# Kernel tuning notes

Measured on AMD Instinct MI355X. Metric: run time of the kernel, lower is better.

## Reference

```python
import jax, jax.numpy as jnp
import numpy as np

B, T, D = 32, 512, 1024
EPS = 1e-12  # torch F.normalize eps


def smooth_l1(x):
    # nn.SmoothL1Loss default beta=1.0
    a = jnp.abs(x)
    return jnp.where(a < 1.0, 0.5 * x * x, a - 0.5)


def setup_inputs() -> dict:
    key = jax.random.key(0)
    k1, k2, k3, k4 = jax.random.split(key, 4)
    return {
        "word_targets": jax.random.normal(k1, (B, T, D), dtype=jnp.float32),
        "image_targets": jax.random.normal(k2, (B, D), dtype=jnp.float32),
        "preds": jax.random.normal(k3, (B, T, D), dtype=jnp.float32),
        "decode_lengths": jax.random.randint(k4, (B,), 1, T + 1, dtype=jnp.int32),
    }


def reference(word_targets, image_targets, preds, decode_lengths):
    # mask over valid (ragged) positions: [B, T]
    mask = (jnp.arange(T)[None, :] < decode_lengths[:, None]).astype(preds.dtype)
    lens = decode_lengths.astype(preds.dtype)  # [B]

    # word loss: per-sample mean of smooth_l1 over valid tokens x D
    sl1 = smooth_l1(preds - word_targets) * mask[:, :, None]  # [B,T,D]
    word_per_b = sl1.sum(axis=(1, 2)) / (lens * D)             # [B]
    word_loss = word_per_b.mean()

    # per-sentence means over valid tokens: [B, D]
    pred_mean = (preds * mask[:, :, None]).sum(axis=1) / lens[:, None]
    targ_mean = (word_targets * mask[:, :, None]).sum(axis=1) / lens[:, None]
    sentence_loss = smooth_l1(pred_mean - targ_mean).mean(axis=1).mean()

    # image embedding loss: compare pred sentence mean to L2-normalized image embedding
    norm = jnp.maximum(jnp.linalg.norm(image_targets, axis=-1, keepdims=True), EPS)
    img_norm = image_targets / norm
    image_loss = smooth_l1(pred_mean - img_norm).mean(axis=1).mean()

    return word_loss + sentence_loss + image_loss
```

## Files before the change

kernel.cpp:

```cpp
#include <hip/hip_runtime.h>
#include <math.h>

static constexpr int B_ = 32;
static constexpr int T_ = 512;
static constexpr int D_ = 1024;
static constexpr int NT_ = 32;
static constexpr int TCHUNK_ = T_ / NT_;
static constexpr int GRID1_ = 1024;
static constexpr float EPS_ = 1e-12f;

__device__ __forceinline__ float sl1f(float x) {
    float a = fabsf(x);
    return a < 1.0f ? 0.5f * x * x : a - 0.5f;
}

__device__ __forceinline__ float blockReduce256(float v, float* lds) {
#pragma unroll
    for (int o = 32; o > 0; o >>= 1) v += __shfl_down(v, o, 64);
    int wid = threadIdx.x >> 6, lane = threadIdx.x & 63;
    if (lane == 0) lds[wid] = v;
    __syncthreads();
    float tot = lds[0] + lds[1] + lds[2] + lds[3];
    __syncthreads();
    return tot;
}

__global__ __launch_bounds__(256, 4) void pass1_kernel(
    const float* __restrict__ preds, const float* __restrict__ wtarg,
    const int* __restrict__ lens,
    float* __restrict__ wsPred, float* __restrict__ wsTarg, float* __restrict__ wsSl1,
    float* __restrict__ out)
{
    __shared__ float lds[4];
    __shared__ int sPrefix[B_ + 1];
    __shared__ int sLen[B_];

    const int tid = threadIdx.x;
    if (blockIdx.x == 0 && tid == 0) out[0] = 0.f;

    if (tid < 64) {
        int len_t = (tid < B_) ? lens[tid] : 0;
        int nc = (len_t + TCHUNK_ - 1) / TCHUNK_;
        int incl = nc;
#pragma unroll
        for (int o = 1; o < 64; o <<= 1) {
            int u = __shfl_up(incl, o, 64);
            if (tid >= o) incl += u;
        }
        if (tid < B_) { sPrefix[tid] = incl - nc; sLen[tid] = len_t; }
        if (tid == B_ - 1) sPrefix[B_] = incl;
    }
    __syncthreads();
    const int total = sPrefix[B_];

    for (int fi = blockIdx.x; fi < total; fi += GRID1_) {
        int lo = 0, hi = B_;
        while (hi - lo > 1) {
            int mid = (lo + hi) >> 1;
            if (sPrefix[mid] <= fi) lo = mid; else hi = mid;
        }
        const int b = lo;
        const int c = fi - sPrefix[lo];
        const int len = sLen[b];
        const int t0 = c * TCHUNK_;
        const int nrows = min(TCHUNK_, len - t0);

        const float4* pp = reinterpret_cast<const float4*>(preds)
                           + (size_t)(b * T_ + t0) * (D_ / 4) + tid;
        const float4* pw = reinterpret_cast<const float4*>(wtarg)
                           + (size_t)(b * T_ + t0) * (D_ / 4) + tid;

        float4 ps = make_float4(0.f, 0.f, 0.f, 0.f);
        float4 ts = make_float4(0.f, 0.f, 0.f, 0.f);
        float s = 0.f;

        if (nrows == TCHUNK_) {
#pragma unroll
            for (int tt = 0; tt < TCHUNK_; tt += 8) {
                float4 p[8], w[8];
#pragma unroll
                for (int j = 0; j < 8; ++j) p[j] = pp[(size_t)(tt + j) * (D_ / 4)];
#pragma unroll
                for (int j = 0; j < 8; ++j) w[j] = pw[(size_t)(tt + j) * (D_ / 4)];
#pragma unroll
                for (int j = 0; j < 8; ++j) {
                    ps.x += p[j].x; ps.y += p[j].y; ps.z += p[j].z; ps.w += p[j].w;
                    ts.x += w[j].x; ts.y += w[j].y; ts.z += w[j].z; ts.w += w[j].w;
                    s += sl1f(p[j].x - w[j].x) + sl1f(p[j].y - w[j].y)
                       + sl1f(p[j].z - w[j].z) + sl1f(p[j].w - w[j].w);
                }
            }
        } else {
            for (int t = 0; t < nrows; ++t) {
                float4 p = pp[(size_t)t * (D_ / 4)];
                float4 w = pw[(size_t)t * (D_ / 4)];
                ps.x += p.x; ps.y += p.y; ps.z += p.z; ps.w += p.w;
                ts.x += w.x; ts.y += w.y; ts.z += w.z; ts.w += w.w;
                s += sl1f(p.x - w.x) + sl1f(p.y - w.y) + sl1f(p.z - w.z) + sl1f(p.w - w.w);
            }
        }

        const size_t off = ((size_t)b * NT_ + c) * (D_ / 4) + tid;
        reinterpret_cast<float4*>(wsPred)[off] = ps;
        reinterpret_cast<float4*>(wsTarg)[off] = ts;

        float tot = blockReduce256(s, lds);
        if (tid == 0) wsSl1[b * NT_ + c] = tot;
    }
}

__global__ __launch_bounds__(256) void pass2_kernel(
    const float* __restrict__ img, const int* __restrict__ lens,
    const float* __restrict__ wsPred, const float* __restrict__ wsTarg,
    const float* __restrict__ wsSl1, float* __restrict__ out)
{
    __shared__ float4 lA[8][32];
    __shared__ float4 lB[8][32];
    __shared__ float lred[4];

    const int g = blockIdx.x, b = blockIdx.y;
    const int tid = threadIdx.x;
    const int c8 = tid >> 5, j = tid & 31;
    const int len = lens[b];
    const float flen = (float)len;
    const int ntmax = (len + TCHUNK_ - 1) / TCHUNK_;

    const float4* img4 = reinterpret_cast<const float4*>(img);
    float4 im = img4[(size_t)b * (D_ / 4) + tid];
    float ss = im.x * im.x + im.y * im.y + im.z * im.z + im.w * im.w;
    float sumsq = blockReduce256(ss, lred);
    float inv_norm = 1.0f / fmaxf(sqrtf(sumsq), EPS_);

    float4 ap = make_float4(0.f, 0.f, 0.f, 0.f);
    float4 at = make_float4(0.f, 0.f, 0.f, 0.f);
#pragma unroll
    for (int k = 0; k < NT_ / 8; ++k) {
        int nt = c8 + k * 8;
        if (nt < ntmax) {
            size_t off = ((size_t)b * NT_ + nt) * (D_ / 4) + (size_t)g * 32 + j;
            float4 p = reinterpret_cast<const float4*>(wsPred)[off];
            float4 w = reinterpret_cast<const float4*>(wsTarg)[off];
            ap.x += p.x; ap.y += p.y; ap.z += p.z; ap.w += p.w;
            at.x += w.x; at.y += w.y; at.z += w.z; at.w += w.w;
        }
    }
    lA[c8][j] = ap;
    lB[c8][j] = at;
    __syncthreads();

    float part = 0.f;
    if (tid < 32) {
        float4 ps = make_float4(0.f, 0.f, 0.f, 0.f);
        float4 ts = make_float4(0.f, 0.f, 0.f, 0.f);
#pragma unroll
        for (int k = 0; k < 8; ++k) {
            float4 p = lA[k][tid], w = lB[k][tid];
            ps.x += p.x; ps.y += p.y; ps.z += p.z; ps.w += p.w;
            ts.x += w.x; ts.y += w.y; ts.z += w.z; ts.w += w.w;
        }
        const float pmx = ps.x / flen, pmy = ps.y / flen, pmz = ps.z / flen, pmw = ps.w / flen;
        const float tmx = ts.x / flen, tmy = ts.y / flen, tmz = ts.z / flen, tmw = ts.w / flen;
        float4 iv = img4[(size_t)b * (D_ / 4) + g * 32 + tid];
        part  = sl1f(pmx - tmx) + sl1f(pmy - tmy) + sl1f(pmz - tmz) + sl1f(pmw - tmw);
        part += sl1f(pmx - iv.x * inv_norm) + sl1f(pmy - iv.y * inv_norm)
              + sl1f(pmz - iv.z * inv_norm) + sl1f(pmw - iv.w * inv_norm);
    }
#pragma unroll
    for (int o = 16; o > 0; o >>= 1) part += __shfl_down(part, o, 64);

    if (tid == 0) {
        float wsum = 0.f;
#pragma unroll
        for (int k = 0; k < NT_ / 8; ++k) {
            int nt = g * (NT_ / 8) + k;
            if (nt < ntmax) wsum += wsSl1[b * NT_ + nt];
        }
        float val = part / (float)D_ + wsum / (flen * (float)D_);
        atomicAdd(out, val * (1.0f / (float)B_));
    }
}

extern "C" void kernel_launch(void* const* d_in, const int* in_sizes, int n_in,
                              void* d_out, int out_size, void* d_ws, size_t ws_size,
                              hipStream_t stream) {
    const float* wtarg = (const float*)d_in[0];
    const float* img   = (const float*)d_in[1];
    const float* preds = (const float*)d_in[2];
    const int*   lens  = (const int*)d_in[3];
    float* out = (float*)d_out;

    float* wsPred = (float*)d_ws;
    float* wsTarg = wsPred + (size_t)B_ * NT_ * D_;
    float* wsSl1  = wsTarg + (size_t)B_ * NT_ * D_;

    pass1_kernel<<<GRID1_, 256, 0, stream>>>(preds, wtarg, lens, wsPred, wsTarg, wsSl1, out);
    pass2_kernel<<<dim3(8, B_), 256, 0, stream>>>(img, lens, wsPred, wsTarg, wsSl1, out);
}
```

Baseline: 24.52 us.

## Accumulate per-sample partial sums with float atomics instead of per-chunk workspace

Pass 1 no longer writes one partial row per time chunk. It atomically adds its column sums and smooth-L1 totals into a compact per-sample workspace, which is zeroed by a memset before launch. Pass 2 becomes one block per sample that reads the final sums directly, with no cross-chunk reduction. This cuts workspace traffic and simplifies pass 2, but adds a memset, contention from many float atomics, and a non-deterministic summation order.

```diff
diff --git a/kernel.cpp b/kernel.cpp
--- a/kernel.cpp
+++ b/kernel.cpp
@@ -28,8 +28,8 @@
 __global__ __launch_bounds__(256, 4) void pass1_kernel(
     const float* __restrict__ preds, const float* __restrict__ wtarg,
     const int* __restrict__ lens,
-    float* __restrict__ wsPred, float* __restrict__ wsTarg, float* __restrict__ wsSl1,
-    float* __restrict__ out)
+    float* __restrict__ wsSumP, float* __restrict__ wsSumT,
+    float* __restrict__ wsWord, float* __restrict__ out)
 {
     __shared__ float lds[4];
     __shared__ int sPrefix[B_ + 1];
@@ -100,30 +100,31 @@
             }
         }
 
-        const size_t off = ((size_t)b * NT_ + c) * (D_ / 4) + tid;
-        reinterpret_cast<float4*>(wsPred)[off] = ps;
-        reinterpret_cast<float4*>(wsTarg)[off] = ts;
+        float* dstP = wsSumP + (size_t)b * D_ + tid * 4;
+        float* dstT = wsSumT + (size_t)b * D_ + tid * 4;
+        unsafeAtomicAdd(dstP + 0, ps.x);
+        unsafeAtomicAdd(dstP + 1, ps.y);
+        unsafeAtomicAdd(dstP + 2, ps.z);
+        unsafeAtomicAdd(dstP + 3, ps.w);
+        unsafeAtomicAdd(dstT + 0, ts.x);
+        unsafeAtomicAdd(dstT + 1, ts.y);
+        unsafeAtomicAdd(dstT + 2, ts.z);
+        unsafeAtomicAdd(dstT + 3, ts.w);
 
         float tot = blockReduce256(s, lds);
-        if (tid == 0) wsSl1[b * NT_ + c] = tot;
+        if (tid == 0) atomicAdd(&wsWord[b], tot);
     }
 }
 
 __global__ __launch_bounds__(256) void pass2_kernel(
     const float* __restrict__ img, const int* __restrict__ lens,
-    const float* __restrict__ wsPred, const float* __restrict__ wsTarg,
-    const float* __restrict__ wsSl1, float* __restrict__ out)
+    const float* __restrict__ wsSumP, const float* __restrict__ wsSumT,
+    const float* __restrict__ wsWord, float* __restrict__ out)
 {
-    __shared__ float4 lA[8][32];
-    __shared__ float4 lB[8][32];
     __shared__ float lred[4];
-
-    const int g = blockIdx.x, b = blockIdx.y;
-    const int tid = threadIdx.x;
-    const int c8 = tid >> 5, j = tid & 31;
+    const int b = blockIdx.x, tid = threadIdx.x;
     const int len = lens[b];
     const float flen = (float)len;
-    const int ntmax = (len + TCHUNK_ - 1) / TCHUNK_;
 
     const float4* img4 = reinterpret_cast<const float4*>(img);
     float4 im = img4[(size_t)b * (D_ / 4) + tid];
@@ -131,52 +132,20 @@
     float sumsq = blockReduce256(ss, lred);
     float inv_norm = 1.0f / fmaxf(sqrtf(sumsq), EPS_);
 
-    float4 ap = make_float4(0.f, 0.f, 0.f, 0.f);
-    float4 at = make_float4(0.f, 0.f, 0.f, 0.f);
-#pragma unroll
-    for (int k = 0; k < NT_ / 8; ++k) {
-        int nt = c8 + k * 8;
-        if (nt < ntmax) {
-            size_t off = ((size_t)b * NT_ + nt) * (D_ / 4) + (size_t)g * 32 + j;
-            float4 p = reinterpret_cast<const float4*>(wsPred)[off];
-            float4 w = reinterpret_cast<const float4*>(wsTarg)[off];
-            ap.x += p.x; ap.y += p.y; ap.z += p.z; ap.w += p.w;
-            at.x += w.x; at.y += w.y; at.z += w.z; at.w += w.w;
-        }
-    }
-    lA[c8][j] = ap;
-    lB[c8][j] = at;
-    __syncthreads();
+    float4 sp = reinterpret_cast<const float4*>(wsSumP)[(size_t)b * (D_ / 4) + tid];
+    float4 st = reinterpret_cast<const float4*>(wsSumT)[(size_t)b * (D_ / 4) + tid];
 
-    float part = 0.f;
-    if (tid < 32) {
-        float4 ps = make_float4(0.f, 0.f, 0.f, 0.f);
-        float4 ts = make_float4(0.f, 0.f, 0.f, 0.f);
-#pragma unroll
-        for (int k = 0; k < 8; ++k) {
-            float4 p = lA[k][tid], w = lB[k][tid];
-            ps.x += p.x; ps.y += p.y; ps.z += p.z; ps.w += p.w;
-            ts.x += w.x; ts.y += w.y; ts.z += w.z; ts.w += w.w;
-        }
-        const float pmx = ps.x / flen, pmy = ps.y / flen, pmz = ps.z / flen, pmw = ps.w / flen;
-        const float tmx = ts.x / flen, tmy = ts.y / flen, tmz = ts.z / flen, tmw = ts.w / flen;
-        float4 iv = img4[(size_t)b * (D_ / 4) + g * 32 + tid];
-        part  = sl1f(pmx - tmx) + sl1f(pmy - tmy) + sl1f(pmz - tmz) + sl1f(pmw - tmw);
-        part += sl1f(pmx - iv.x * inv_norm) + sl1f(pmy - iv.y * inv_norm)
-              + sl1f(pmz - iv.z * inv_norm) + sl1f(pmw - iv.w * inv_norm);
-    }
-#pragma unroll
-    for (int o = 16; o > 0; o >>= 1) part += __shfl_down(part, o, 64);
+    const float pmx = sp.x / flen, pmy = sp.y / flen, pmz = sp.z / flen, pmw = sp.w / flen;
+    const float tmx = st.x / flen, tmy = st.y / flen, tmz = st.z / flen, tmw = st.w / flen;
+
+    float s = sl1f(pmx - tmx) + sl1f(pmy - tmy) + sl1f(pmz - tmz) + sl1f(pmw - tmw)
+            + sl1f(pmx - im.x * inv_norm) + sl1f(pmy - im.y * inv_norm)
+            + sl1f(pmz - im.z * inv_norm) + sl1f(pmw - im.w * inv_norm);
+    float tot = blockReduce256(s, lred);
 
     if (tid == 0) {
-        float wsum = 0.f;
-#pragma unroll
-        for (int k = 0; k < NT_ / 8; ++k) {
-            int nt = g * (NT_ / 8) + k;
-            if (nt < ntmax) wsum += wsSl1[b * NT_ + nt];
-        }
-        float val = part / (float)D_ + wsum / (flen * (float)D_);
-        atomicAdd(out, val * (1.0f / (float)B_));
+        float per_b = tot / (float)D_ + wsWord[b] / (flen * (float)D_);
+        atomicAdd(out, per_b * (1.0f / (float)B_));
     }
 }
 
@@ -189,10 +158,14 @@
     const int*   lens  = (const int*)d_in[3];
     float* out = (float*)d_out;
 
-    float* wsPred = (float*)d_ws;
-    float* wsTarg = wsPred + (size_t)B_ * NT_ * D_;
-    float* wsSl1  = wsTarg + (size_t)B_ * NT_ * D_;
+    float* wsSumP = (float*)d_ws;
+    float* wsSumT = wsSumP + (size_t)B_ * D_;
+    float* wsWord = wsSumT + (size_t)B_ * D_;
 
-    pass1_kernel<<<GRID1_, 256, 0, stream>>>(preds, wtarg, lens, wsPred, wsTarg, wsSl1, out);
-    pass2_kernel<<<dim3(8, B_), 256, 0, stream>>>(img, lens, wsPred, wsTarg, wsSl1, out);
+    const size_t zero_bytes = ((size_t)2 * B_ * D_ + B_) * sizeof(float);
+    hipMemsetAsync(d_ws, 0, zero_bytes, stream);
+
+    pass1_kernel<<<GRID1_, 256, 0, stream>>>(preds, wtarg, lens,
+                                             wsSumP, wsSumT, wsWord, out);
+    pass2_kernel<<<B_, 256, 0, stream>>>(img, lens, wsSumP, wsSumT, wsWord, out);
 }
```

After: 41.91 us. 70.9% more time.
